# Kernel optimization log

Measured on AMD Instinct MI355X. Metric: run time of the kernel, lower is better.

## Reference

```python
import jax, jax.numpy as jnp
import numpy as np

HIDDEN = 4096
N_HEADS = 32
N_KV_HEADS = 8
HEAD_DIM = HIDDEN // N_HEADS  # 128
N_GROUPS = N_HEADS // N_KV_HEADS  # 4
ROPE_THETA = 10000.0


def setup_inputs() -> dict:
    key = jax.random.key(0)
    k1, k2, k3, k4, k5 = jax.random.split(key, 5)
    B, S = 2, 2048
    hidden_states = jax.random.normal(k1, (B, S, HIDDEN), dtype=jnp.float32)
    position_ids = jnp.arange(S, dtype=jnp.int64 if jax.config.jax_enable_x64 else jnp.int32)[None, :]
    scale = 0.02
    Wq = jax.random.normal(k2, (N_HEADS * HEAD_DIM, HIDDEN), dtype=jnp.float32) * scale
    Wk = jax.random.normal(k3, (N_KV_HEADS * HEAD_DIM, HIDDEN), dtype=jnp.float32) * scale
    Wv = jax.random.normal(k4, (N_KV_HEADS * HEAD_DIM, HIDDEN), dtype=jnp.float32) * scale
    Wo = jax.random.normal(k5, (HIDDEN, N_HEADS * HEAD_DIM), dtype=jnp.float32) * scale
    return {"hidden_states": hidden_states, "position_ids": position_ids,
            "Wq": Wq, "Wk": Wk, "Wv": Wv, "Wo": Wo}


def _rope_cos_sin(position_ids, dtype):
    # inv_freq: [HEAD_DIM/2]
    inv_freq = 1.0 / (ROPE_THETA ** (jnp.arange(0, HEAD_DIM, 2, dtype=jnp.float32) / HEAD_DIM))
    freqs = position_ids.astype(jnp.float32)[..., None] * inv_freq  # [1, S, D/2]
    emb = jnp.concatenate([freqs, freqs], axis=-1)                  # [1, S, D]
    return jnp.cos(emb).astype(dtype), jnp.sin(emb).astype(dtype)


def _rotate_half(x):
    x1, x2 = jnp.split(x, 2, axis=-1)
    return jnp.concatenate([-x2, x1], axis=-1)


def reference(hidden_states, position_ids, Wq, Wk, Wv, Wo):
    B, S, H = hidden_states.shape
    d = HEAD_DIM
    # projections -> [B, heads, S, d]
    q = (hidden_states @ Wq.T).reshape(B, S, N_HEADS, d).transpose(0, 2, 1, 3)
    k = (hidden_states @ Wk.T).reshape(B, S, N_KV_HEADS, d).transpose(0, 2, 1, 3)
    v = (hidden_states @ Wv.T).reshape(B, S, N_KV_HEADS, d).transpose(0, 2, 1, 3)
    cos, sin = _rope_cos_sin(position_ids, q.dtype)  # [1, S, d]
    cos, sin = cos[:, None], sin[:, None]            # [1, 1, S, d]
    q = q * cos + _rotate_half(q) * sin
    k = k * cos + _rotate_half(k) * sin
    # GQA: group query heads over shared kv heads (no explicit expand)
    qg = q.reshape(B, N_KV_HEADS, N_GROUPS, S, d)
    scores = jnp.einsum('bkgqd,bkld->bkgql', qg, k) / jnp.sqrt(jnp.asarray(d, q.dtype))
    w = jax.nn.softmax(scores, axis=-1)  # NOTE: no causal mask, matching source
    o = jnp.einsum('bkgql,bkld->bkgqd', w, v)        # [B, kvh, g, S, d]
    o = o.reshape(B, N_HEADS, S, d).transpose(0, 2, 1, 3).reshape(B, S, N_HEADS * d)
    return o @ Wo.T
```

## Files before the change

kernel.cpp:

```cpp
#include <hip/hip_runtime.h>
#include <math.h>

#define HIDDEN 4096
#define NH 32
#define NKV 8
#define HD 128
#define BBATCH 2
#define SEQ 2048
#define BS 4096
#define QKVD 6144

typedef __attribute__((ext_vector_type(8))) short short8;
typedef __attribute__((ext_vector_type(4))) float f32x4;
typedef __attribute__((ext_vector_type(4))) unsigned int uint4v;

__device__ __forceinline__ unsigned short f2bf(float f) {
  union { float f; unsigned int u; } v; v.f = f;
  unsigned int r = v.u + 0x7fffu + ((v.u >> 16) & 1u);
  return (unsigned short)(r >> 16);
}
__device__ __forceinline__ float bf2f(unsigned short u) {
  union { unsigned int u; float f; } v; v.u = ((unsigned int)u) << 16;
  return v.f;
}
__device__ __forceinline__ unsigned int cvtpk(float lo, float hi) {
  unsigned int r;
  asm("v_cvt_pk_bf16_f32 %0, %1, %2" : "=v"(r) : "v"(lo), "v"(hi));
  return r;
}

__device__ __forceinline__ void gload16(const unsigned short* g, unsigned short* l) {
  __builtin_amdgcn_global_load_lds((const __attribute__((address_space(1))) unsigned int*)(const void*)g,
                                   (__attribute__((address_space(3))) unsigned int*)(void*)l, 16, 0, 0);
}

__global__ void cast_f32_bf16(const float* __restrict__ in, unsigned short* __restrict__ out) {
  int i = (blockIdx.x * blockDim.x + threadIdx.x) * 4;
  float4 f = *(const float4*)(in + i);
  ushort4 u;
  u.x = f2bf(f.x); u.y = f2bf(f.y); u.z = f2bf(f.z); u.w = f2bf(f.w);
  *(ushort4*)(out + i) = u;
}

template<int OUT_F32>
__global__ __launch_bounds__(256) void gemm_bt128(const unsigned short* __restrict__ A,
                                                  const unsigned short* __restrict__ Bm,
                                                  void* __restrict__ Cc,
                                                  int M, int N, int K) {
  __shared__ unsigned short As[128 * 32];
  __shared__ unsigned short Bs[128 * 32];
  int t = threadIdx.x, lane = t & 63, wave = t >> 6;
  int lm = lane & 15, quad = lane >> 4;
  int wm = wave >> 1, wn = wave & 1;
  int m0 = blockIdx.y * 128, n0 = blockIdx.x * 128;
  int srow = t >> 2;
  int pcol = (((t & 3) ^ (srow & 3)) * 8);
  f32x4 acc[4][4] = {};
  const unsigned short* ag = A + (size_t)(m0 + srow) * K + pcol;
  const unsigned short* bg = Bm + (size_t)(n0 + srow) * K + pcol;
  unsigned short* asl = &As[(size_t)t * 8];
  unsigned short* bsl = &Bs[(size_t)t * 8];
  for (int k0 = 0; k0 < K; k0 += 32) {
    __syncthreads();
    gload16(ag + k0, asl);
    gload16(ag + (size_t)64 * K + k0, asl + 2048);
    gload16(bg + k0, bsl);
    gload16(bg + (size_t)64 * K + k0, bsl + 2048);
    __syncthreads();
    int xq = (quad ^ (lm & 3)) * 8;
    short8 af[4], bf[4];
#pragma unroll
    for (int mt = 0; mt < 4; mt++)
      af[mt] = *(const short8*)&As[(wm * 64 + mt * 16 + lm) * 32 + xq];
#pragma unroll
    for (int nt = 0; nt < 4; nt++)
      bf[nt] = *(const short8*)&Bs[(wn * 64 + nt * 16 + lm) * 32 + xq];
#pragma unroll
    for (int mt = 0; mt < 4; mt++)
#pragma unroll
      for (int nt = 0; nt < 4; nt++)
        acc[mt][nt] = __builtin_amdgcn_mfma_f32_16x16x32_bf16(af[mt], bf[nt], acc[mt][nt], 0, 0, 0);
  }
#pragma unroll
  for (int mt = 0; mt < 4; mt++)
#pragma unroll
    for (int nt = 0; nt < 4; nt++)
#pragma unroll
      for (int r = 0; r < 4; r++) {
        size_t row = m0 + wm * 64 + mt * 16 + quad * 4 + r;
        size_t col = n0 + wn * 64 + nt * 16 + lm;
        if (OUT_F32) ((float*)Cc)[row * N + col] = acc[mt][nt][r];
        else ((unsigned short*)Cc)[row * N + col] = f2bf(acc[mt][nt][r]);
      }
}

__global__ void rope_kernel(unsigned short* __restrict__ x, const int* __restrict__ pos_ids,
                            int nheads, int rstride) {
  int idx = blockIdx.x * blockDim.x + threadIdx.x;
  int j = idx & 63;
  int h = (idx >> 6) % nheads;
  int row = idx / (64 * nheads);
  int s = row & (SEQ - 1);
  float p = (float)pos_ids[s];
  float inv = exp2f(-(float)j * (13.287712379549449f / 64.0f));
  float f = p * inv;
  float c = cosf(f), sn = sinf(f);
  unsigned short* ptr = x + (size_t)row * rstride + h * HD;
  float x1 = bf2f(ptr[j]), x2 = bf2f(ptr[j + 64]);
  ptr[j]      = f2bf(x1 * c - x2 * sn);
  ptr[j + 64] = f2bf(x2 * c + x1 * sn);
}

__global__ void transpose_v(const unsigned short* __restrict__ v, unsigned short* __restrict__ vt) {
  int idx = blockIdx.x * blockDim.x + threadIdx.x;
  int s = idx & (SEQ - 1);
  int d = (idx >> 11) & (HD - 1);
  int kv = (idx >> 18) & (NKV - 1);
  int b = idx >> 21;
  vt[idx] = v[((size_t)(b * SEQ + s)) * QKVD + kv * HD + d];
}

__global__ __launch_bounds__(256) void attn_kernel(const unsigned short* __restrict__ Q,
                                                   const unsigned short* __restrict__ Kb,
                                                   const unsigned short* __restrict__ Vt,
                                                   unsigned short* __restrict__ O) {
  __shared__ unsigned short Ks[64 * 136];
  __shared__ unsigned short Vs[128 * 72];
  int t = threadIdx.x, wave = t >> 6, lane = t & 63;
  int lm = lane & 15, quad = lane >> 4;
  int blk0 = blockIdx.x;
  int blk = (blk0 & 7) * 128 + (blk0 >> 3);
  int qt = blk & 15;
  int h = (blk >> 4) & 31;
  int b = blk >> 9;
  int kv = h >> 2;
  int qs0 = qt * 128 + wave * 32;
  const float c = 0.08838834764831845f * 1.4426950408889634f;

  short8 aq[2][4];
#pragma unroll
  for (int s = 0; s < 2; s++) {
    const unsigned short* qbase = Q + ((size_t)(b * SEQ + qs0 + s * 16 + lm)) * QKVD + h * HD;
#pragma unroll
    for (int kk = 0; kk < 4; kk++)
      aq[s][kk] = *(const short8*)(qbase + kk * 32 + quad * 8);
  }

  f32x4 acc[2][8] = {};
  float mrow[2] = {-1e30f, -1e30f};
  float lrow[2] = {0.f, 0.f};
  const unsigned short* kbase = Kb + (size_t)b * SEQ * QKVD + kv * HD;
  const unsigned short* vbase = Vt + ((size_t)(b * NKV + kv)) * HD * SEQ;

  int krow = t >> 4, kcol = (t & 15) * 8;
  int vrow = t >> 3, vcol = (t & 7) * 8;
  int keyr[4];
#pragma unroll
  for (int pp = 0; pp < 4; pp++) {
    int srow = pp * 16 + krow;
    keyr[pp] = (srow & 0x20) | ((srow & 0x0C) << 1) | ((srow & 0x10) >> 2) | (srow & 3);
  }

  for (int kblk = 0; kblk < SEQ; kblk += 64) {
#pragma unroll
    for (int pp = 0; pp < 4; pp++) {
      *(uint4*)&Ks[(pp * 16 + krow) * 136 + kcol] =
          *(const uint4*)(kbase + (size_t)(kblk + keyr[pp]) * QKVD + kcol);
      *(uint4*)&Vs[(pp * 32 + vrow) * 72 + vcol] =
          *(const uint4*)(vbase + (size_t)(pp * 32 + vrow) * SEQ + kblk + vcol);
    }
    __syncthreads();
    f32x4 sc[2][4] = {};
    __builtin_amdgcn_s_setprio(1);
#pragma unroll
    for (int kt = 0; kt < 4; kt++) {
#pragma unroll
      for (int kk = 0; kk < 4; kk++) {
        short8 bk = *(const short8*)&Ks[(kt * 16 + lm) * 136 + kk * 32 + quad * 8];
        sc[0][kt] = __builtin_amdgcn_mfma_f32_16x16x32_bf16(bk, aq[0][kk], sc[0][kt], 0, 0, 0);
        sc[1][kt] = __builtin_amdgcn_mfma_f32_16x16x32_bf16(bk, aq[1][kk], sc[1][kt], 0, 0, 0);
      }
    }
    __builtin_amdgcn_s_setprio(0);
    union PW { uint4v w; short8 h; } pw[2][2];
#pragma unroll
    for (int s = 0; s < 2; s++) {
      float vmax = -1e30f;
#pragma unroll
      for (int kt = 0; kt < 4; kt++)
        vmax = fmaxf(vmax, fmaxf(fmaxf(sc[s][kt][0], sc[s][kt][1]),
                                 fmaxf(sc[s][kt][2], sc[s][kt][3])));
      vmax *= c;
      vmax = fmaxf(vmax, __shfl_xor(vmax, 16));
      vmax = fmaxf(vmax, __shfl_xor(vmax, 32));
      if (__any(vmax > mrow[s] + 8.0f)) {
        float nm = fmaxf(mrow[s], vmax);
        float alpha = __builtin_amdgcn_exp2f(mrow[s] - nm);
        mrow[s] = nm;
        lrow[s] *= alpha;
#pragma unroll
        for (int r = 0; r < 4; r++) {
          float ar = __shfl(alpha, quad * 4 + r);
#pragma unroll
          for (int tt = 0; tt < 8; tt++) acc[s][tt][r] *= ar;
        }
      }
      float nm = mrow[s];
      float rs = 0.f;
#pragma unroll
      for (int kt = 0; kt < 4; kt++) {
        float p0 = __builtin_amdgcn_exp2f(sc[s][kt][0] * c - nm);
        float p1 = __builtin_amdgcn_exp2f(sc[s][kt][1] * c - nm);
        float p2 = __builtin_amdgcn_exp2f(sc[s][kt][2] * c - nm);
        float p3 = __builtin_amdgcn_exp2f(sc[s][kt][3] * c - nm);
        rs += (p0 + p1) + (p2 + p3);
        pw[s][kt >> 1].w[(kt & 1) * 2 + 0] = cvtpk(p0, p1);
        pw[s][kt >> 1].w[(kt & 1) * 2 + 1] = cvtpk(p2, p3);
      }
      rs += __shfl_xor(rs, 16);
      rs += __shfl_xor(rs, 32);
      lrow[s] += rs;
    }
    __builtin_amdgcn_s_setprio(1);
#pragma unroll
    for (int g = 0; g < 2; g++) {
      short8 ap0 = pw[0][g].h;
      short8 ap1 = pw[1][g].h;
#pragma unroll
      for (int tt = 0; tt < 8; tt++) {
        short8 bv = *(const short8*)&Vs[(tt * 16 + lm) * 72 + g * 32 + quad * 8];
        acc[0][tt] = __builtin_amdgcn_mfma_f32_16x16x32_bf16(ap0, bv, acc[0][tt], 0, 0, 0);
        acc[1][tt] = __builtin_amdgcn_mfma_f32_16x16x32_bf16(ap1, bv, acc[1][tt], 0, 0, 0);
      }
    }
    __builtin_amdgcn_s_setprio(0);
    __syncthreads();
  }
#pragma unroll
  for (int s = 0; s < 2; s++) {
#pragma unroll
    for (int r = 0; r < 4; r++) {
      float lq = __shfl(lrow[s], quad * 4 + r);
      float inv = 1.0f / lq;
      int row = qs0 + s * 16 + quad * 4 + r;
      unsigned short* op = O + ((size_t)(b * SEQ + row)) * HIDDEN + h * HD;
#pragma unroll
      for (int tt = 0; tt < 8; tt++)
        op[tt * 16 + lm] = f2bf(acc[s][tt][r] * inv);
    }
  }
}

extern "C" void kernel_launch(void* const* d_in, const int* in_sizes, int n_in,
                              void* d_out, int out_size, void* d_ws, size_t ws_size,
                              hipStream_t stream) {
  const float* hidden = (const float*)d_in[0];
  const int*   pos    = (const int*)d_in[1];
  const float* Wq     = (const float*)d_in[2];
  const float* Wk     = (const float*)d_in[3];
  const float* Wv     = (const float*)d_in[4];
  const float* Wo     = (const float*)d_in[5];

  char* ws = (char*)d_ws;
  unsigned short* hx  = (unsigned short*)ws; ws += (size_t)BS * HIDDEN * 2;
  unsigned short* wq  = (unsigned short*)ws; ws += (size_t)HIDDEN * HIDDEN * 2;
  unsigned short* wk  = (unsigned short*)ws; ws += (size_t)1024 * HIDDEN * 2;
  unsigned short* wv  = (unsigned short*)ws; ws += (size_t)1024 * HIDDEN * 2;
  unsigned short* wo  = (unsigned short*)ws; ws += (size_t)HIDDEN * HIDDEN * 2;
  unsigned short* qkv = (unsigned short*)ws; ws += (size_t)BS * QKVD * 2;
  unsigned short* vt  = (unsigned short*)ws; ws += (size_t)BS * 1024 * 2;
  unsigned short* ob  = (unsigned short*)ws; ws += (size_t)BS * HIDDEN * 2;

  cast_f32_bf16<<<16384, 256, 0, stream>>>(hidden, hx);
  cast_f32_bf16<<<16384, 256, 0, stream>>>(Wq, wq);
  cast_f32_bf16<<<4096, 256, 0, stream>>>(Wk, wk);
  cast_f32_bf16<<<4096, 256, 0, stream>>>(Wv, wv);
  cast_f32_bf16<<<16384, 256, 0, stream>>>(Wo, wo);
  gemm_bt128<0><<<dim3(48, 32), 256, 0, stream>>>(hx, wq, qkv, BS, QKVD, HIDDEN);
  rope_kernel<<<32768, 256, 0, stream>>>(qkv, pos, NH, QKVD);
  rope_kernel<<<8192, 256, 0, stream>>>(qkv + HIDDEN, pos, NKV, QKVD);
  transpose_v<<<16384, 256, 0, stream>>>(qkv + HIDDEN + 1024, vt);
  attn_kernel<<<1024, 256, 0, stream>>>(qkv, qkv + HIDDEN, vt, ob);
  gemm_bt128<1><<<dim3(32, 32), 256, 0, stream>>>(ob, wo, d_out, BS, HIDDEN, HIDDEN);
}
```

Baseline: 1.009 ms.

## Double-buffer attention K/V via direct LDS loads, fuse casts and rope, tile V transpose

The attention kernel now double-buffers K and V tiles in LDS. It fills them with global_load_lds and an XOR swizzle in place of padded rows, so the next block's loads overlap the current block's MFMA work. The five cast launches are merged into one kernel. The two RoPE launches become one pass over Q and K heads that reads a precomputed cos/sin table. The V transpose now goes through a shared-memory tile with 16-byte stores instead of strided scalar gathers. Together these aim to cut launch overhead, redundant trig work and uncoalesced memory traffic, at the cost of more LDS per attention block and more complex swizzle indexing.

```diff
diff --git a/kernel.cpp b/kernel.cpp
--- a/kernel.cpp
+++ b/kernel.cpp
@@ -34,12 +34,23 @@
                                    (__attribute__((address_space(3))) unsigned int*)(void*)l, 16, 0, 0);
 }
 
-__global__ void cast_f32_bf16(const float* __restrict__ in, unsigned short* __restrict__ out) {
-  int i = (blockIdx.x * blockDim.x + threadIdx.x) * 4;
-  float4 f = *(const float4*)(in + i);
+__global__ void cast_all(const float* __restrict__ h, const float* __restrict__ q,
+                         const float* __restrict__ k, const float* __restrict__ v,
+                         const float* __restrict__ o,
+                         unsigned short* hx, unsigned short* wq, unsigned short* wk,
+                         unsigned short* wv, unsigned short* wo) {
+  int b = blockIdx.x;
+  const float* src; unsigned short* dst; int base;
+  if (b < 16384)      { src = h; dst = hx; base = 0; }
+  else if (b < 32768) { src = q; dst = wq; base = 16384; }
+  else if (b < 36864) { src = k; dst = wk; base = 32768; }
+  else if (b < 40960) { src = v; dst = wv; base = 36864; }
+  else                { src = o; dst = wo; base = 40960; }
+  size_t i = ((size_t)(b - base) * 256 + threadIdx.x) * 4;
+  float4 f = *(const float4*)(src + i);
   ushort4 u;
   u.x = f2bf(f.x); u.y = f2bf(f.y); u.z = f2bf(f.z); u.w = f2bf(f.w);
-  *(ushort4*)(out + i) = u;
+  *(ushort4*)(dst + i) = u;
 }
 
 template<int OUT_F32>
@@ -94,38 +105,58 @@
       }
 }
 
-__global__ void rope_kernel(unsigned short* __restrict__ x, const int* __restrict__ pos_ids,
-                            int nheads, int rstride) {
+__global__ void build_rope_table(const int* __restrict__ pos, float2* __restrict__ cs) {
+  int idx = blockIdx.x * blockDim.x + threadIdx.x;
+  int j = idx & 63, s = idx >> 6;
+  float p = (float)pos[s];
+  float f = p * exp2f(-(float)j * (13.287712379549449f / 64.0f));
+  cs[idx] = make_float2(cosf(f), sinf(f));
+}
+
+__global__ void rope_fused(unsigned short* __restrict__ x, const float2* __restrict__ cs) {
   int idx = blockIdx.x * blockDim.x + threadIdx.x;
   int j = idx & 63;
-  int h = (idx >> 6) % nheads;
-  int row = idx / (64 * nheads);
+  int q6 = idx >> 6;
+  int hh = q6 % 40;
+  int row = q6 / 40;
   int s = row & (SEQ - 1);
-  float p = (float)pos_ids[s];
-  float inv = exp2f(-(float)j * (13.287712379549449f / 64.0f));
-  float f = p * inv;
-  float c = cosf(f), sn = sinf(f);
-  unsigned short* ptr = x + (size_t)row * rstride + h * HD;
+  float2 t2 = cs[(s << 6) | j];
+  unsigned short* ptr = x + (size_t)row * QKVD + hh * HD;
   float x1 = bf2f(ptr[j]), x2 = bf2f(ptr[j + 64]);
-  ptr[j]      = f2bf(x1 * c - x2 * sn);
-  ptr[j + 64] = f2bf(x2 * c + x1 * sn);
+  ptr[j]      = f2bf(x1 * t2.x - x2 * t2.y);
+  ptr[j + 64] = f2bf(x2 * t2.x + x1 * t2.y);
 }
 
 __global__ void transpose_v(const unsigned short* __restrict__ v, unsigned short* __restrict__ vt) {
-  int idx = blockIdx.x * blockDim.x + threadIdx.x;
-  int s = idx & (SEQ - 1);
-  int d = (idx >> 11) & (HD - 1);
-  int kv = (idx >> 18) & (NKV - 1);
-  int b = idx >> 21;
-  vt[idx] = v[((size_t)(b * SEQ + s)) * QKVD + kv * HD + d];
+  __shared__ unsigned short tile[64][72];
+  int bx = blockIdx.x;
+  int s0 = (bx & 31) * 64;
+  int d0 = ((bx >> 5) & 1) * 64;
+  int bk = bx >> 6;
+  int b = bk >> 3, kv = bk & 7;
+  int t = threadIdx.x;
+  int rs = t >> 2, rc = (t & 3) * 16;
+  const unsigned short* src = v + ((size_t)(b * SEQ + s0 + rs)) * QKVD + kv * HD + d0 + rc;
+  *(uint4*)&tile[rs][rc]     = *(const uint4*)src;
+  *(uint4*)&tile[rs][rc + 8] = *(const uint4*)(src + 8);
+  __syncthreads();
+  int wd = t >> 2, wc = (t & 3) * 16;
+  short8 o0, o1;
+#pragma unroll
+  for (int e = 0; e < 8; e++) o0[e] = (short)tile[wc + e][wd];
+#pragma unroll
+  for (int e = 0; e < 8; e++) o1[e] = (short)tile[wc + 8 + e][wd];
+  unsigned short* dst = vt + ((size_t)bk * HD + d0 + wd) * SEQ + s0 + wc;
+  *(short8*)dst = o0;
+  *(short8*)(dst + 8) = o1;
 }
 
 __global__ __launch_bounds__(256) void attn_kernel(const unsigned short* __restrict__ Q,
                                                    const unsigned short* __restrict__ Kb,
                                                    const unsigned short* __restrict__ Vt,
                                                    unsigned short* __restrict__ O) {
-  __shared__ unsigned short Ks[64 * 136];
-  __shared__ unsigned short Vs[128 * 72];
+  __shared__ unsigned short Ksh[2 * 64 * 128];
+  __shared__ unsigned short Vsh[2 * 128 * 64];
   int t = threadIdx.x, wave = t >> 6, lane = t & 63;
   int lm = lane & 15, quad = lane >> 4;
   int blk0 = blockIdx.x;
@@ -152,31 +183,58 @@
   const unsigned short* kbase = Kb + (size_t)b * SEQ * QKVD + kv * HD;
   const unsigned short* vbase = Vt + ((size_t)(b * NKV + kv)) * HD * SEQ;
 
-  int krow = t >> 4, kcol = (t & 15) * 8;
-  int vrow = t >> 3, vcol = (t & 7) * 8;
-  int keyr[4];
-#pragma unroll
-  for (int pp = 0; pp < 4; pp++) {
-    int srow = pp * 16 + krow;
-    keyr[pp] = (srow & 0x20) | ((srow & 0x0C) << 1) | ((srow & 0x10) >> 2) | (srow & 3);
-  }
-
-  for (int kblk = 0; kblk < SEQ; kblk += 64) {
-#pragma unroll
-    for (int pp = 0; pp < 4; pp++) {
-      *(uint4*)&Ks[(pp * 16 + krow) * 136 + kcol] =
-          *(const uint4*)(kbase + (size_t)(kblk + keyr[pp]) * QKVD + kcol);
-      *(uint4*)&Vs[(pp * 32 + vrow) * 72 + vcol] =
-          *(const uint4*)(vbase + (size_t)(pp * 32 + vrow) * SEQ + kblk + vcol);
-    }
-    __syncthreads();
+  int trow = t >> 4;
+  int kchunk = (t & 15) ^ (trow & 7);
+  const unsigned short* ksrc[4];
+#pragma unroll
+  for (int i = 0; i < 4; i++) {
+    int srow = i * 16 + trow;
+    int key = (srow & 0x20) | ((srow & 0x0C) << 1) | ((srow & 0x10) >> 2) | (srow & 3);
+    ksrc[i] = kbase + (size_t)key * QKVD + kchunk * 8;
+  }
+  int vrow = t >> 3;
+  int vchunk = (t & 7) ^ (vrow & 7);
+  const unsigned short* vsrc[4];
+#pragma unroll
+  for (int i = 0; i < 4; i++)
+    vsrc[i] = vbase + (size_t)(i * 32 + vrow) * SEQ + vchunk * 8;
+
+  int xr8 = (lm & 7) * 8;
+
+  {
+    unsigned short* kd = Ksh + t * 8;
+    unsigned short* vd = Vsh + t * 8;
+#pragma unroll
+    for (int i = 0; i < 4; i++) gload16(ksrc[i], kd + i * 2048);
+#pragma unroll
+    for (int i = 0; i < 4; i++) gload16(vsrc[i], vd + i * 2048);
+#pragma unroll
+    for (int i = 0; i < 4; i++) { ksrc[i] += 64 * QKVD; vsrc[i] += 64; }
+  }
+  asm volatile("s_waitcnt vmcnt(0)" ::: "memory");
+  __syncthreads();
+
+  int cur = 0;
+  for (int it = 0; it < SEQ / 64; it++) {
+    if (it < SEQ / 64 - 1) {
+      unsigned short* kd = Ksh + (cur ^ 1) * 8192 + t * 8;
+      unsigned short* vd = Vsh + (cur ^ 1) * 8192 + t * 8;
+#pragma unroll
+      for (int i = 0; i < 4; i++) gload16(ksrc[i], kd + i * 2048);
+#pragma unroll
+      for (int i = 0; i < 4; i++) gload16(vsrc[i], vd + i * 2048);
+#pragma unroll
+      for (int i = 0; i < 4; i++) { ksrc[i] += 64 * QKVD; vsrc[i] += 64; }
+    }
+    const unsigned short* kcur = Ksh + cur * 8192;
+    const unsigned short* vcur = Vsh + cur * 8192;
     f32x4 sc[2][4] = {};
     __builtin_amdgcn_s_setprio(1);
 #pragma unroll
     for (int kt = 0; kt < 4; kt++) {
 #pragma unroll
       for (int kk = 0; kk < 4; kk++) {
-        short8 bk = *(const short8*)&Ks[(kt * 16 + lm) * 136 + kk * 32 + quad * 8];
+        short8 bk = *(const short8*)&kcur[(kt * 16 + lm) * 128 + (((kk * 4 + quad) * 8) ^ xr8)];
         sc[0][kt] = __builtin_amdgcn_mfma_f32_16x16x32_bf16(bk, aq[0][kk], sc[0][kt], 0, 0, 0);
         sc[1][kt] = __builtin_amdgcn_mfma_f32_16x16x32_bf16(bk, aq[1][kk], sc[1][kt], 0, 0, 0);
       }
@@ -228,13 +286,15 @@
       short8 ap1 = pw[1][g].h;
 #pragma unroll
       for (int tt = 0; tt < 8; tt++) {
-        short8 bv = *(const short8*)&Vs[(tt * 16 + lm) * 72 + g * 32 + quad * 8];
+        short8 bv = *(const short8*)&vcur[(tt * 16 + lm) * 64 + (((g * 4 + quad) * 8) ^ xr8)];
         acc[0][tt] = __builtin_amdgcn_mfma_f32_16x16x32_bf16(ap0, bv, acc[0][tt], 0, 0, 0);
         acc[1][tt] = __builtin_amdgcn_mfma_f32_16x16x32_bf16(ap1, bv, acc[1][tt], 0, 0, 0);
       }
     }
     __builtin_amdgcn_s_setprio(0);
+    asm volatile("s_waitcnt vmcnt(0)" ::: "memory");
     __syncthreads();
+    cur ^= 1;
   }
 #pragma unroll
   for (int s = 0; s < 2; s++) {
@@ -270,16 +330,13 @@
   unsigned short* qkv = (unsigned short*)ws; ws += (size_t)BS * QKVD * 2;
   unsigned short* vt  = (unsigned short*)ws; ws += (size_t)BS * 1024 * 2;
   unsigned short* ob  = (unsigned short*)ws; ws += (size_t)BS * HIDDEN * 2;
-
-  cast_f32_bf16<<<16384, 256, 0, stream>>>(hidden, hx);
-  cast_f32_bf16<<<16384, 256, 0, stream>>>(Wq, wq);
-  cast_f32_bf16<<<4096, 256, 0, stream>>>(Wk, wk);
-  cast_f32_bf16<<<4096, 256, 0, stream>>>(Wv, wv);
-  cast_f32_bf16<<<16384, 256, 0, stream>>>(Wo, wo);
+  float2*         cs  = (float2*)ws;         ws += (size_t)SEQ * 64 * sizeof(float2);
+
+  build_rope_table<<<512, 256, 0, stream>>>(pos, cs);
+  cast_all<<<57344, 256, 0, stream>>>(hidden, Wq, Wk, Wv, Wo, hx, wq, wk, wv, wo);
   gemm_bt128<0><<<dim3(48, 32), 256, 0, stream>>>(hx, wq, qkv, BS, QKVD, HIDDEN);
-  rope_kernel<<<32768, 256, 0, stream>>>(qkv, pos, NH, QKVD);
-  rope_kernel<<<8192, 256, 0, stream>>>(qkv + HIDDEN, pos, NKV, QKVD);
-  transpose_v<<<16384, 256, 0, stream>>>(qkv + HIDDEN + 1024, vt);
+  rope_fused<<<40960, 256, 0, stream>>>(qkv, cs);
+  transpose_v<<<1024, 256, 0, stream>>>(qkv + HIDDEN + 1024, vt);
   attn_kernel<<<1024, 256, 0, stream>>>(qkv, qkv + HIDDEN, vt, ob);
   gemm_bt128<1><<<dim3(32, 32), 256, 0, stream>>>(ob, wo, d_out, BS, HIDDEN, HIDDEN);
 }
```

After: 892.5 us. 11.6% less time.
